# Performance work log

Hardware: AMD Instinct MI355X
Metric: run time of the kernel (lower is better)

## Reference

```python
import jax, jax.numpy as jnp
import numpy as np

B, S, D, H = 4, 2048, 1024, 16
DK = D // H


def setup_inputs() -> dict:
    key = jax.random.key(0)
    ks = jax.random.split(key, 12)
    std = 0.02
    inp = {
        "query": jax.random.normal(ks[0], (B, S, D), jnp.float32),
        "key": jax.random.normal(ks[1], (B, S, D), jnp.float32),
        "value": jax.random.normal(ks[2], (B, S, D), jnp.float32),
        "mask": jnp.ones((B, 1, 1, S), jnp.int32),
        "Wq": jax.random.normal(ks[3], (D, D), jnp.float32) * std,
        "bq": jnp.zeros((D,), jnp.float32),
        "Wk": jax.random.normal(ks[4], (D, D), jnp.float32) * std,
        "bk": jnp.zeros((D,), jnp.float32),
        "Wv": jax.random.normal(ks[5], (D, D), jnp.float32) * std,
        "bv": jnp.zeros((D,), jnp.float32),
        "Wo": jax.random.normal(ks[6], (D, D), jnp.float32) * std,
        "bo": jnp.zeros((D,), jnp.float32),
    }
    return inp


def reference(query, key, value, mask, Wq, bq, Wk, bk, Wv, bv, Wo, bo):
    # nn.Linear: x @ W.T + b; then split heads -> [B, H, S, DK]
    def proj(x, W, b):
        y = x @ W.T + b
        return y.reshape(B, S, H, DK).transpose(0, 2, 1, 3)

    q = proj(query, Wq, bq)
    k = proj(key, Wk, bk)
    v = proj(value, Wv, bv)

    scale = 1.0 / jnp.sqrt(jnp.asarray(DK, q.dtype))
    scores = jnp.einsum('bhqd,bhkd->bhqk', q, k) * scale  # [B,H,S,S]
    scores = jnp.where(mask == 0, jnp.asarray(-1e9, scores.dtype), scores)
    p_attn = jax.nn.softmax(scores, axis=-1)  # dropout p=0 -> identity
    ctx = jnp.einsum('bhqk,bhkd->bhqd', p_attn, v)
    ctx = ctx.transpose(0, 2, 1, 3).reshape(B, S, D)
    out = ctx @ Wo.T + bo
    return out
```

## Files before the change

### kernel.cpp

```cpp
#include <hip/hip_runtime.h>

#define BB 4
#define SS 2048
#define DD 1024
#define HH 16
#define DKC 64
#define MT (BB*SS)
#define NX (MT*DD)
#define NW (DD*DD)

typedef _Float16 f16x8 __attribute__((ext_vector_type(8)));
typedef _Float16 f16x4 __attribute__((ext_vector_type(4)));
typedef float f32x4 __attribute__((ext_vector_type(4)));
typedef int   i32x4 __attribute__((ext_vector_type(4)));
typedef unsigned u32x4 __attribute__((ext_vector_type(4)));

__global__ __launch_bounds__(256) void cvt_all(const float* __restrict__ xq,
                                               const float* __restrict__ xk,
                                               const float* __restrict__ xv,
                                               const float* __restrict__ wq,
                                               const float* __restrict__ wk,
                                               const float* __restrict__ wv,
                                               const float* __restrict__ wo,
                                               _Float16* __restrict__ dst) {
  size_t i = ((size_t)blockIdx.x * 256 + threadIdx.x) * 4;
  const float* src; size_t off;
  if (i < (size_t)NX)          { src = xq; off = i; }
  else if (i < (size_t)2*NX)   { src = xk; off = i - (size_t)NX; }
  else if (i < (size_t)3*NX)   { src = xv; off = i - (size_t)2*NX; }
  else {
    size_t j = i - (size_t)3*NX;
    if (j < (size_t)NW)        { src = wq; off = j; }
    else if (j < (size_t)2*NW) { src = wk; off = j - (size_t)NW; }
    else if (j < (size_t)3*NW) { src = wv; off = j - (size_t)2*NW; }
    else                       { src = wo; off = j - (size_t)3*NW; }
  }
  f32x4 f = *(const f32x4*)(src + off);
  f16x4 o;
#pragma unroll
  for (int j = 0; j < 4; ++j) o[j] = (_Float16)f[j];
  *(f16x4*)(dst + i) = o;
}

__global__ __launch_bounds__(256) void gemm_qkv(const _Float16* __restrict__ Xb,
                                                const _Float16* __restrict__ Wb,
                                                const float* __restrict__ b0,
                                                const float* __restrict__ b1,
                                                const float* __restrict__ b2,
                                                _Float16* __restrict__ Pj) {
  const int z = blockIdx.z;
  const _Float16* A = Xb + (size_t)z * MT * DD;
  const _Float16* W = Wb + (size_t)z * DD * DD;
  const float* bias = (z == 0) ? b0 : ((z == 1) ? b1 : b2);
  _Float16* out = Pj + (size_t)z * MT * DD;

  const int m0 = blockIdx.x * 128;
  const int n0 = blockIdx.y * 128;
  const int t = threadIdx.x;
  const int lane = t & 63;
  const int wave = t >> 6;
  const int q = lane >> 4, r = lane & 15;
  const int wm = (wave & 1) * 64, wn = (wave >> 1) * 64;

  __shared__ __align__(16) _Float16 sA[128 * 32];
  __shared__ __align__(16) _Float16 sB[128 * 32];

  f32x4 acc[4][4] = {};

  const int row0 = t >> 2, cc = t & 3;
  const int wch = (t & 3) ^ ((t >> 3) & 3);
  const int fsw = (r >> 1) & 3;

  f16x8 apre[2], bpre[2];

  auto prefetch = [&](int k0) {
#pragma unroll
    for (int i = 0; i < 2; ++i) {
      int row = row0 + 64 * i;
      apre[i] = *(const f16x8*)(A + (size_t)(m0 + row) * DD + k0 + cc * 8);
      bpre[i] = *(const f16x8*)(W + (size_t)(n0 + row) * DD + k0 + cc * 8);
    }
  };

  prefetch(0);

  for (int k0 = 0; k0 < DD; k0 += 32) {
#pragma unroll
    for (int i = 0; i < 2; ++i) {
      int row = row0 + 64 * i;
      *(f16x8*)&sA[row * 32 + wch * 8] = apre[i];
      *(f16x8*)&sB[row * 32 + wch * 8] = bpre[i];
    }
    __syncthreads();
    if (k0 + 32 < DD) prefetch(k0 + 32);

    f16x8 af[4], bf[4];
#pragma unroll
    for (int x = 0; x < 4; ++x) {
      af[x] = *(const f16x8*)&sA[(wm + x * 16 + r) * 32 + ((q ^ fsw) * 8)];
      bf[x] = *(const f16x8*)&sB[(wn + x * 16 + r) * 32 + ((q ^ fsw) * 8)];
    }
#pragma unroll
    for (int mi = 0; mi < 4; ++mi)
#pragma unroll
      for (int ni = 0; ni < 4; ++ni)
        acc[mi][ni] = __builtin_amdgcn_mfma_f32_16x16x32_f16(af[mi], bf[ni], acc[mi][ni], 0, 0, 0);
    __syncthreads();
  }

  if (z == 2) {
    int s_tile = (m0 + wm) & 2047;
    int bb2 = (m0 + wm) >> 11;
#pragma unroll
    for (int ni = 0; ni < 4; ++ni) {
      int gn = n0 + wn + ni * 16 + r;
      float bv = bias[gn];
      int hh = gn >> 6, dk = gn & 63;
      size_t base = ((size_t)((bb2 * HH + hh) * DKC + dk)) * SS + s_tile;
#pragma unroll
      for (int mi = 0; mi < 4; ++mi) {
        int kap0 = 4 * (mi & 1) + 8 * q + 32 * (mi >> 1);
        f16x4 o4;
#pragma unroll
        for (int rr = 0; rr < 4; ++rr) o4[rr] = (_Float16)(acc[mi][ni][rr] + bv);
        *(f16x4*)&out[base + kap0] = o4;
      }
    }
  } else {
    int hh = (n0 + wn) >> 6;
    float bv4[4];
#pragma unroll
    for (int ni = 0; ni < 4; ++ni) bv4[ni] = bias[n0 + wn + ni * 16 + r];
#pragma unroll
    for (int mi = 0; mi < 4; ++mi) {
#pragma unroll
      for (int rr = 0; rr < 4; ++rr) {
        int gm = m0 + wm + mi * 16 + q * 4 + rr;
        int bb2 = gm >> 11, s = gm & 2047;
        f16x4 o4;
#pragma unroll
        for (int ni = 0; ni < 4; ++ni) o4[ni] = (_Float16)(acc[mi][ni][rr] + bv4[ni]);
        *(f16x4*)&out[((size_t)((bb2 * HH + hh) * SS + s)) * DKC + r * 4] = o4;
      }
    }
  }
}

__global__ __launch_bounds__(256) void attn(const _Float16* __restrict__ Pj,
                                            const int* __restrict__ mask,
                                            _Float16* __restrict__ Cx) {
  const int qt = blockIdx.x, h = blockIdx.y, bb = blockIdx.z;
  const size_t hoff = ((size_t)(bb * HH + h) * SS) * DKC;
  const _Float16* Qh  = Pj + hoff;
  const _Float16* Kh  = Pj + (size_t)MT * DD + hoff;
  const _Float16* Vth = Pj + (size_t)2 * MT * DD + hoff;
  _Float16* Ch = Cx + hoff;
  const int* mrow = mask + bb * SS;

  const int t = threadIdx.x, lane = t & 63, wave = t >> 6;
  const int q = lane >> 4, r = lane & 15;
  const int qrow0 = qt * 128 + wave * 32;

  __shared__ __align__(16) _Float16 sK[64 * 64];
  __shared__ __align__(16) _Float16 sVt[64 * 64];
  __shared__ __align__(16) _Float16 sMBh[SS];

  {
    int i0 = t * 8;
    i32x4 m0v = *(const i32x4*)(mrow + i0);
    i32x4 m1v = *(const i32x4*)(mrow + i0 + 4);
    f16x8 bvv;
#pragma unroll
    for (int j = 0; j < 4; ++j) {
      bvv[j]     = m0v[j] ? (_Float16)0.0f : (_Float16)(-30000.0f);
      bvv[4 + j] = m1v[j] ? (_Float16)0.0f : (_Float16)(-30000.0f);
    }
    *(f16x8*)&sMBh[i0] = bvv;
  }

  f16x8 qf[2][2];
#pragma unroll
  for (int n = 0; n < 2; ++n)
#pragma unroll
    for (int kk = 0; kk < 2; ++kk)
      qf[n][kk] = *(const f16x8*)&Qh[(size_t)(qrow0 + n * 16 + r) * DKC + kk * 32 + q * 8];

  float lst[2] = {};
  f32x4 oacc[2][4] = {};

  const float C2 = 0.125f * 1.44269504089f;

  const int srow0 = t >> 3, scc = t & 7;

  f16x8 kpre[2], vpre[2];
#pragma unroll
  for (int i = 0; i < 2; ++i) {
    int row = srow0 + 32 * i;
    kpre[i] = *(const f16x8*)(Kh + (size_t)row * DKC + scc * 8);
    vpre[i] = *(const f16x8*)(Vth + (size_t)row * SS + scc * 8);
  }

  for (int kt = 0; kt < SS; kt += 64) {
#pragma unroll
    for (int i = 0; i < 2; ++i) {
      int row = srow0 + 32 * i;
      *(f16x8*)&sK [row * 64 + ((scc ^ (row & 7)) << 3)] = kpre[i];
      *(f16x8*)&sVt[row * 64 + ((scc ^ (row & 7)) << 3)] = vpre[i];
    }
    __syncthreads();

    if (kt + 64 < SS) {
#pragma unroll
      for (int i = 0; i < 2; ++i) {
        int row = srow0 + 32 * i;
        kpre[i] = *(const f16x8*)(Kh + (size_t)(kt + 64 + row) * DKC + scc * 8);
        vpre[i] = *(const f16x8*)(Vth + (size_t)row * SS + kt + 64 + scc * 8);
      }
    }

    f32x4 sacc[4][2] = {};
#pragma unroll
    for (int kk = 0; kk < 2; ++kk) {
      f16x8 kb[4];
#pragma unroll
      for (int a = 0; a < 4; ++a)
        kb[a] = *(const f16x8*)&sK[(a * 16 + r) * 64 + (((kk * 4 + q) ^ (r & 7)) << 3)];
      __builtin_amdgcn_s_setprio(1);
#pragma unroll
      for (int a = 0; a < 4; ++a)
#pragma unroll
        for (int n = 0; n < 2; ++n)
          sacc[a][n] = __builtin_amdgcn_mfma_f32_16x16x32_f16(kb[a], qf[n][kk], sacc[a][n], 0, 0, 0);
      __builtin_amdgcn_s_setprio(0);
    }

    f16x4 mbv[4];
#pragma unroll
    for (int a = 0; a < 4; ++a)
      mbv[a] = *(const f16x4*)&sMBh[kt + a * 16 + q * 4];

    unsigned pw[2][2][4];
#pragma unroll
    for (int n = 0; n < 2; ++n) {
#pragma unroll
      for (int a = 0; a < 4; ++a) {
        float pp[4];
#pragma unroll
        for (int reg = 0; reg < 4; ++reg)
          pp[reg] = __builtin_amdgcn_exp2f(__builtin_fmaf(sacc[a][n][reg], C2, (float)mbv[a][reg]));
        lst[n] += (pp[0] + pp[1]) + (pp[2] + pp[3]);
        pw[n][a >> 1][(a & 1) * 2]     = __builtin_bit_cast(unsigned, __builtin_amdgcn_cvt_pkrtz(pp[0], pp[1]));
        pw[n][a >> 1][(a & 1) * 2 + 1] = __builtin_bit_cast(unsigned, __builtin_amdgcn_cvt_pkrtz(pp[2], pp[3]));
      }
    }

#pragma unroll
    for (int kk = 0; kk < 2; ++kk) {
      f16x8 vb[4];
#pragma unroll
      for (int ni = 0; ni < 4; ++ni)
        vb[ni] = *(const f16x8*)&sVt[(ni * 16 + r) * 64 + (((kk * 4 + q) ^ (r & 7)) << 3)];
      __builtin_amdgcn_s_setprio(1);
#pragma unroll
      for (int n = 0; n < 2; ++n) {
        u32x4 w = { pw[n][kk][0], pw[n][kk][1], pw[n][kk][2], pw[n][kk][3] };
        f16x8 apn = __builtin_bit_cast(f16x8, w);
#pragma unroll
        for (int ni = 0; ni < 4; ++ni)
          oacc[n][ni] = __builtin_amdgcn_mfma_f32_16x16x32_f16(apn, vb[ni], oacc[n][ni], 0, 0, 0);
      }
      __builtin_amdgcn_s_setprio(0);
    }
    __syncthreads();
  }

  float rinv[2];
#pragma unroll
  for (int n = 0; n < 2; ++n) {
    float l = lst[n];
    l += __shfl_xor(l, 16);
    l += __shfl_xor(l, 32);
    rinv[n] = 1.0f / l;
  }
  float rn[2][4];
#pragma unroll
  for (int n = 0; n < 2; ++n)
#pragma unroll
    for (int rr = 0; rr < 4; ++rr)
      rn[n][rr] = __shfl(rinv[n], q * 4 + rr);

#pragma unroll
  for (int mi = 0; mi < 2; ++mi)
#pragma unroll
    for (int ni = 0; ni < 4; ++ni)
#pragma unroll
      for (int rr = 0; rr < 4; ++rr) {
        int row = qrow0 + mi * 16 + q * 4 + rr;
        Ch[(size_t)row * DKC + ni * 16 + r] = (_Float16)(oacc[mi][ni][rr] * rn[mi][rr]);
      }
}

__global__ __launch_bounds__(256) void gemm_out(const _Float16* __restrict__ Cx,
                                                const _Float16* __restrict__ W,
                                                const float* __restrict__ bias,
                                                float* __restrict__ out) {
  const int m0 = blockIdx.x * 128;
  const int n0 = blockIdx.y * 128;
  const int t = threadIdx.x;
  const int lane = t & 63;
  const int wave = t >> 6;
  const int q = lane >> 4, r = lane & 15;
  const int wm = (wave & 1) * 64, wn = (wave >> 1) * 64;

  __shared__ __align__(16) _Float16 sA[128 * 32];
  __shared__ __align__(16) _Float16 sB[128 * 32];

  f32x4 acc[4][4] = {};

  const int row0 = t >> 2, cc = t & 3;
  const int wch = (t & 3) ^ ((t >> 3) & 3);
  const int fsw = (r >> 1) & 3;

  size_t abase[2];
#pragma unroll
  for (int i = 0; i < 2; ++i) {
    int gm = m0 + row0 + 64 * i;
    int bb = gm >> 11, s = gm & 2047;
    abase[i] = ((size_t)(bb * HH) * SS + s) * DKC;
  }

  f16x8 apre[2], bpre[2];

  auto prefetch = [&](int k0) {
    int head = k0 >> 6, off = (k0 & 63) + cc * 8;
#pragma unroll
    for (int i = 0; i < 2; ++i) {
      apre[i] = *(const f16x8*)(Cx + abase[i] + (size_t)head * SS * DKC + off);
      bpre[i] = *(const f16x8*)(W + (size_t)(n0 + row0 + 64 * i) * DD + k0 + cc * 8);
    }
  };

  prefetch(0);

  for (int k0 = 0; k0 < DD; k0 += 32) {
#pragma unroll
    for (int i = 0; i < 2; ++i) {
      int row = row0 + 64 * i;
      *(f16x8*)&sA[row * 32 + wch * 8] = apre[i];
      *(f16x8*)&sB[row * 32 + wch * 8] = bpre[i];
    }
    __syncthreads();
    if (k0 + 32 < DD) prefetch(k0 + 32);

    f16x8 af[4], bf[4];
#pragma unroll
    for (int x = 0; x < 4; ++x) {
      af[x] = *(const f16x8*)&sA[(wm + x * 16 + r) * 32 + ((q ^ fsw) * 8)];
      bf[x] = *(const f16x8*)&sB[(wn + x * 16 + r) * 32 + ((q ^ fsw) * 8)];
    }
#pragma unroll
    for (int mi = 0; mi < 4; ++mi)
#pragma unroll
      for (int ni = 0; ni < 4; ++ni)
        acc[mi][ni] = __builtin_amdgcn_mfma_f32_16x16x32_f16(af[mi], bf[ni], acc[mi][ni], 0, 0, 0);
    __syncthreads();
  }

#pragma unroll
  for (int ni = 0; ni < 4; ++ni) {
    int gn = n0 + wn + ni * 16 + r;
    float bv = bias[gn];
#pragma unroll
    for (int mi = 0; mi < 4; ++mi) {
#pragma unroll
      for (int rr = 0; rr < 4; ++rr) {
        int gm = m0 + wm + mi * 16 + q * 4 + rr;
        out[(size_t)gm * DD + gn] = acc[mi][ni][rr] + bv;
      }
    }
  }
}

extern "C" void kernel_launch(void* const* d_in, const int* in_sizes, int n_in,
                              void* d_out, int out_size, void* d_ws, size_t ws_size,
                              hipStream_t stream) {
  const float* query = (const float*)d_in[0];
  const float* key_  = (const float*)d_in[1];
  const float* value = (const float*)d_in[2];
  const int*   mask  = (const int*)d_in[3];
  const float* Wq = (const float*)d_in[4];
  const float* bq = (const float*)d_in[5];
  const float* Wk = (const float*)d_in[6];
  const float* bk = (const float*)d_in[7];
  const float* Wv = (const float*)d_in[8];
  const float* bv = (const float*)d_in[9];
  const float* Wo = (const float*)d_in[10];
  const float* bo = (const float*)d_in[11];
  float* out = (float*)d_out;

  _Float16* Xb = (_Float16*)d_ws;
  _Float16* Wb = Xb + (size_t)3 * NX;
  _Float16* Pj = Wb + (size_t)4 * NW;
  _Float16* Cx = Pj + (size_t)3 * NX;

  cvt_all<<<(3 * NX + 4 * NW) / 1024, 256, 0, stream>>>(query, key_, value, Wq, Wk, Wv, Wo, Xb);

  gemm_qkv<<<dim3(MT / 128, DD / 128, 3), 256, 0, stream>>>(Xb, Wb, bq, bk, bv, Pj);
  attn<<<dim3(SS / 128, HH, BB), 256, 0, stream>>>(Pj, mask, Cx);
  gemm_out<<<dim3(MT / 128, DD / 128), 256, 0, stream>>>(Cx, Wb + (size_t)3 * NW, bo, out);
}
```

Baseline: 346.7 us.

## Remap blocks for XCD L2 locality and double-buffer attention K/V tiles

Both GEMM kernels and the attention kernel now remap block IDs so that blocks sharing operands (the same M rows, or the same head's K/V) land on the same XCD, improving L2 reuse across MI355X's chiplets. The attention kernel also double-buffers its K/V shared-memory tiles. The next tile is stored into the alternate buffer after compute, which removes one barrier per iteration in exchange for twice the LDS footprint.

```diff
diff --git a/kernel.cpp b/kernel.cpp
--- a/kernel.cpp
+++ b/kernel.cpp
@@ -54,8 +54,11 @@
   const float* bias = (z == 0) ? b0 : ((z == 1) ? b1 : b2);
   _Float16* out = Pj + (size_t)z * MT * DD;
 
-  const int m0 = blockIdx.x * 128;
-  const int n0 = blockIdx.y * 128;
+  const int bid = blockIdx.y * 64 + blockIdx.x;
+  const int xcd = bid & 7, idx = bid >> 3;
+  const int m0 = (xcd * 8 + (idx & 7)) * 128;
+  const int n0 = (idx >> 3) * 128;
+
   const int t = threadIdx.x;
   const int lane = t & 63;
   const int wave = t >> 6;
@@ -149,7 +152,10 @@
 __global__ __launch_bounds__(256) void attn(const _Float16* __restrict__ Pj,
                                             const int* __restrict__ mask,
                                             _Float16* __restrict__ Cx) {
-  const int qt = blockIdx.x, h = blockIdx.y, bb = blockIdx.z;
+  const int d = blockIdx.x;
+  const int w = (d & 7) * 128 + (d >> 3);
+  const int qt = w & 15, hb = w >> 4;
+  const int h = hb & 15, bb = hb >> 4;
   const size_t hoff = ((size_t)(bb * HH + h) * SS) * DKC;
   const _Float16* Qh  = Pj + hoff;
   const _Float16* Kh  = Pj + (size_t)MT * DD + hoff;
@@ -161,8 +167,8 @@
   const int q = lane >> 4, r = lane & 15;
   const int qrow0 = qt * 128 + wave * 32;
 
-  __shared__ __align__(16) _Float16 sK[64 * 64];
-  __shared__ __align__(16) _Float16 sVt[64 * 64];
+  __shared__ __align__(16) _Float16 sK[2][64 * 64];
+  __shared__ __align__(16) _Float16 sVt[2][64 * 64];
   __shared__ __align__(16) _Float16 sMBh[SS];
 
   {
@@ -193,30 +199,31 @@
   const int srow0 = t >> 3, scc = t & 7;
 
   f16x8 kpre[2], vpre[2];
+
 #pragma unroll
   for (int i = 0; i < 2; ++i) {
     int row = srow0 + 32 * i;
     kpre[i] = *(const f16x8*)(Kh + (size_t)row * DKC + scc * 8);
     vpre[i] = *(const f16x8*)(Vth + (size_t)row * SS + scc * 8);
   }
+#pragma unroll
+  for (int i = 0; i < 2; ++i) {
+    int row = srow0 + 32 * i;
+    *(f16x8*)&sK [0][row * 64 + ((scc ^ (row & 7)) << 3)] = kpre[i];
+    *(f16x8*)&sVt[0][row * 64 + ((scc ^ (row & 7)) << 3)] = vpre[i];
+  }
+#pragma unroll
+  for (int i = 0; i < 2; ++i) {
+    int row = srow0 + 32 * i;
+    kpre[i] = *(const f16x8*)(Kh + (size_t)(64 + row) * DKC + scc * 8);
+    vpre[i] = *(const f16x8*)(Vth + (size_t)row * SS + 64 + scc * 8);
+  }
+  __syncthreads();
 
   for (int kt = 0; kt < SS; kt += 64) {
-#pragma unroll
-    for (int i = 0; i < 2; ++i) {
-      int row = srow0 + 32 * i;
-      *(f16x8*)&sK [row * 64 + ((scc ^ (row & 7)) << 3)] = kpre[i];
-      *(f16x8*)&sVt[row * 64 + ((scc ^ (row & 7)) << 3)] = vpre[i];
-    }
-    __syncthreads();
-
-    if (kt + 64 < SS) {
-#pragma unroll
-      for (int i = 0; i < 2; ++i) {
-        int row = srow0 + 32 * i;
-        kpre[i] = *(const f16x8*)(Kh + (size_t)(kt + 64 + row) * DKC + scc * 8);
-        vpre[i] = *(const f16x8*)(Vth + (size_t)row * SS + kt + 64 + scc * 8);
-      }
-    }
+    const int cur = (kt >> 6) & 1;
+    const _Float16* sKc = sK[cur];
+    const _Float16* sVc = sVt[cur];
 
     f32x4 sacc[4][2] = {};
 #pragma unroll
@@ -224,7 +231,7 @@
       f16x8 kb[4];
 #pragma unroll
       for (int a = 0; a < 4; ++a)
-        kb[a] = *(const f16x8*)&sK[(a * 16 + r) * 64 + (((kk * 4 + q) ^ (r & 7)) << 3)];
+        kb[a] = *(const f16x8*)&sKc[(a * 16 + r) * 64 + (((kk * 4 + q) ^ (r & 7)) << 3)];
       __builtin_amdgcn_s_setprio(1);
 #pragma unroll
       for (int a = 0; a < 4; ++a)
@@ -259,17 +266,34 @@
       f16x8 vb[4];
 #pragma unroll
       for (int ni = 0; ni < 4; ++ni)
-        vb[ni] = *(const f16x8*)&sVt[(ni * 16 + r) * 64 + (((kk * 4 + q) ^ (r & 7)) << 3)];
+        vb[ni] = *(const f16x8*)&sVc[(ni * 16 + r) * 64 + (((kk * 4 + q) ^ (r & 7)) << 3)];
       __builtin_amdgcn_s_setprio(1);
 #pragma unroll
       for (int n = 0; n < 2; ++n) {
-        u32x4 w = { pw[n][kk][0], pw[n][kk][1], pw[n][kk][2], pw[n][kk][3] };
-        f16x8 apn = __builtin_bit_cast(f16x8, w);
+        u32x4 ww = { pw[n][kk][0], pw[n][kk][1], pw[n][kk][2], pw[n][kk][3] };
+        f16x8 apn = __builtin_bit_cast(f16x8, ww);
 #pragma unroll
         for (int ni = 0; ni < 4; ++ni)
           oacc[n][ni] = __builtin_amdgcn_mfma_f32_16x16x32_f16(apn, vb[ni], oacc[n][ni], 0, 0, 0);
       }
       __builtin_amdgcn_s_setprio(0);
+    }
+
+    if (kt + 64 < SS) {
+#pragma unroll
+      for (int i = 0; i < 2; ++i) {
+        int row = srow0 + 32 * i;
+        *(f16x8*)&sK [cur ^ 1][row * 64 + ((scc ^ (row & 7)) << 3)] = kpre[i];
+        *(f16x8*)&sVt[cur ^ 1][row * 64 + ((scc ^ (row & 7)) << 3)] = vpre[i];
+      }
+      if (kt + 128 < SS) {
+#pragma unroll
+        for (int i = 0; i < 2; ++i) {
+          int row = srow0 + 32 * i;
+          kpre[i] = *(const f16x8*)(Kh + (size_t)(kt + 128 + row) * DKC + scc * 8);
+          vpre[i] = *(const f16x8*)(Vth + (size_t)row * SS + kt + 128 + scc * 8);
+        }
+      }
     }
     __syncthreads();
   }
@@ -304,8 +328,11 @@
                                                 const _Float16* __restrict__ W,
                                                 const float* __restrict__ bias,
                                                 float* __restrict__ out) {
-  const int m0 = blockIdx.x * 128;
-  const int n0 = blockIdx.y * 128;
+  const int bid = blockIdx.y * 64 + blockIdx.x;
+  const int xcd = bid & 7, idx = bid >> 3;
+  const int m0 = (xcd * 8 + (idx & 7)) * 128;
+  const int n0 = (idx >> 3) * 128;
+
   const int t = threadIdx.x;
   const int lane = t & 63;
   const int wave = t >> 6;
@@ -406,6 +433,6 @@
   cvt_all<<<(3 * NX + 4 * NW) / 1024, 256, 0, stream>>>(query, key_, value, Wq, Wk, Wv, Wo, Xb);
 
   gemm_qkv<<<dim3(MT / 128, DD / 128, 3), 256, 0, stream>>>(Xb, Wb, bq, bk, bv, Pj);
-  attn<<<dim3(SS / 128, HH, BB), 256, 0, stream>>>(Pj, mask, Cx);
+  attn<<<dim3((SS / 128) * HH * BB), 256, 0, stream>>>(Pj, mask, Cx);
   gemm_out<<<dim3(MT / 128, DD / 128), 256, 0, stream>>>(Cx, Wb + (size_t)3 * NW, bo, out);
 }
```

After: 373.3 us. 7.7% more time.
